# Kernel tuning notes

Hardware: AMD Instinct MI355X
Metric: run time of the kernel (lower is better)

The kernel has to match this reference:

```python
import jax, jax.numpy as jnp
import numpy as np
import math

N_NODES = 50000
N_EDGES = 800000
IN_DIM = 128
OUT_DIM = 64
TIME_DIM = 128


def setup_inputs() -> dict:
    key = jax.random.key(0)
    ks = jax.random.split(key, 9)
    return {
        "node_feats": jax.random.normal(ks[0], (N_NODES, IN_DIM), dtype=jnp.float32),
        "time_diff": jax.random.uniform(ks[1], (N_EDGES,), dtype=jnp.float32),
        "src": jax.random.randint(ks[2], (N_EDGES,), 0, N_NODES, dtype=jnp.int32),
        "dst": jax.random.randint(ks[3], (N_EDGES,), 0, N_NODES, dtype=jnp.int32),
        "W": jax.random.normal(ks[4], (OUT_DIM, IN_DIM), dtype=jnp.float32) * 0.05,
        "Wv": jax.random.normal(ks[5], (OUT_DIM, IN_DIM), dtype=jnp.float32) * 0.05,
        "omega": jax.random.normal(ks[6], (TIME_DIM // 2,), dtype=jnp.float32),
        "Wt": jax.random.normal(ks[7], (OUT_DIM, TIME_DIM), dtype=jnp.float32) * 0.05,
        "a": jax.random.normal(ks[8], (3 * OUT_DIM,), dtype=jnp.float32) * 0.05,
    }


def reference(node_feats, time_diff, src, dst, W, Wv, omega, Wt, a):
    N = node_feats.shape[0]
    d = W.shape[0]  # out_dim
    time_dim = 2 * omega.shape[0]

    # gather + linear projections per edge
    h_src = node_feats[src] @ W.T          # [E, d]
    h_dst = node_feats[dst] @ W.T          # [E, d]
    v_src = node_feats[src] @ Wv.T         # [E, d]

    # temporal encoding: interleaved sin/cos of t * omega, scaled by sqrt(1/dim)
    ang = time_diff[:, None] * omega[None, :]                       # [E, dim/2]
    pe = jnp.stack([jnp.sin(ang), jnp.cos(ang)], axis=-1)
    pe = pe.reshape(ang.shape[0], time_dim) * jnp.float32(math.sqrt(1.0 / time_dim))
    t_emb = pe @ Wt.T                                               # [E, d]

    # attn_fc(concat([h_src, h_dst, t_emb])) == split dot products (same math, no big concat)
    e = h_src @ a[:d] + h_dst @ a[d:2 * d] + t_emb @ a[2 * d:]      # [E]
    e = jnp.where(e > 0, e, 0.2 * e)  # LeakyReLU(0.2)

    # edge_softmax: softmax over incoming edges of each destination node
    m = jax.ops.segment_max(e, dst, num_segments=N)
    ex = jnp.exp(e - m[dst])
    den = jax.ops.segment_sum(ex, dst, num_segments=N)
    alpha = ex / den[dst]  # dropout is identity in eval mode

    # weighted message scatter-sum aggregation
    msg = v_src * alpha[:, None]                                    # [E, d]
    return jax.ops.segment_sum(msg, dst, num_segments=N)            # [N, d]
```

## Files before the change

### kernel.cpp

```cpp
#include <hip/hip_runtime.h>
#include <hip/hip_bf16.h>
#include <hip/hip_fp16.h>
#include <math.h>

#define IN_DIM   128
#define OUT_DIM  64
#define THALF    64
#define PE_SCALE 0.08838834764831845f
#define TBL      2048
#define EPB_LOG  14
#define EPB      (1 << EPB_LOG)

typedef __attribute__((ext_vector_type(8))) short  short8;
typedef __attribute__((ext_vector_type(4))) float  f32x4;

__device__ inline unsigned short bf16_rne(float x) {
    unsigned u = __float_as_uint(x);
    return (unsigned short)((u + 0x7FFFu + ((u >> 16) & 1u)) >> 16);
}

__global__ __launch_bounds__(256) void k_prep(
    const float* __restrict__ W, const float* __restrict__ Wt,
    const float* __restrict__ a, const float* __restrict__ Wv,
    const float* __restrict__ omega,
    float* __restrict__ gtab, unsigned short* __restrict__ Bp,
    int* __restrict__ pref)
{
    __shared__ float satv[IN_DIM];
    __shared__ float saW1[IN_DIM], saW2[IN_DIM];
    int t = threadIdx.x;
    if (t < IN_DIM) {
        float x3 = 0.f;
        for (int j = 0; j < OUT_DIM; ++j)
            x3 += a[2 * OUT_DIM + j] * Wt[j * IN_DIM + t];
        satv[t] = x3;
        if (blockIdx.x == 0) {
            float x1 = 0.f, x2 = 0.f;
            for (int j = 0; j < OUT_DIM; ++j) {
                float wj = W[j * IN_DIM + t];
                x1 += a[j] * wj;
                x2 += a[OUT_DIM + j] * wj;
            }
            saW1[t] = x1; saW2[t] = x2;
        }
    }
    __syncthreads();

    int idx = blockIdx.x * 256 + t;
    if (idx <= TBL) {
        float tt = (float)idx * (1.0f / TBL);
        float acc = 0.f;
#pragma unroll
        for (int i = 0; i < THALF; ++i) {
            float sp, cp;
            __sincosf(tt * omega[i], &sp, &cp);
            acc += sp * satv[2 * i] + cp * satv[2 * i + 1];
        }
        gtab[idx] = acc;
    }
    if (idx < 64) pref[idx] = 0;

    if (blockIdx.x == 0) {
        for (int i = t; i < 5 * 4 * 64 * 8; i += 256) {
            int j    = i & 7;
            int lane = (i >> 3) & 63;
            int k0i  = (i >> 9) & 3;
            int tt   = i >> 11;
            int kk = k0i * 32 + (lane >> 4) * 8 + j;
            int n  = lane & 15;
            float val;
            if (tt < 4)     val = Wv[(tt * 16 + n) * IN_DIM + kk];
            else            val = (n == 0) ? saW1[kk] : (n == 1) ? saW2[kk] : 0.f;
            Bp[i] = bf16_rne(val);
        }
    }
}

__global__ __launch_bounds__(1024) void k_hist_mfma(
    const int* __restrict__ dst,
    unsigned short* __restrict__ lrank,
    unsigned short* __restrict__ ghist16,
    const float* __restrict__ feats,
    const unsigned short* __restrict__ Bp,
    unsigned short* __restrict__ vb,
    float* __restrict__ s1,
    float* __restrict__ s2,
    int N, int E, int B)
{
    extern __shared__ unsigned h[];
    int t = threadIdx.x;
    if ((int)blockIdx.x < B) {
        int NH = (N + 1) >> 1;
        for (int i = t; i < NH; i += 1024) h[i] = 0u;
        __syncthreads();
        int b = blockIdx.x;
        int e0 = b << EPB_LOG;
        int e1 = e0 + EPB; if (e1 > E) e1 = E;
        for (int e = e0 + t; e < e1; e += 1024) {
            int d = dst[e];
            unsigned inc = (d & 1) ? 0x10000u : 1u;
            unsigned old = atomicAdd(&h[d >> 1], inc);
            lrank[e] = (unsigned short)((d & 1) ? (old >> 16) : (old & 0xFFFFu));
        }
        __syncthreads();
        unsigned* gh32 = (unsigned*)(ghist16 + (size_t)b * N);
        for (int w = t; w < NH; w += 1024) gh32[w] = h[w];
        return;
    }
    int gwave = ((int)blockIdx.x - B) * 16 + (t >> 6);
    int lane  = t & 63;
    int ntiles = (N + 15) >> 4;
    if (gwave >= ntiles) return;
    int row = lane & 15, quad = lane >> 4;
    int nodeA = gwave * 16 + row;
    int nodeL = nodeA < N ? nodeA : N - 1;

    const float* arow = feats + (size_t)nodeL * IN_DIM + quad * 8;
    short8 afrag[4];
#pragma unroll
    for (int k0i = 0; k0i < 4; ++k0i) {
        float4 fa = *(const float4*)(arow + k0i * 32);
        float4 fb = *(const float4*)(arow + k0i * 32 + 4);
        union { unsigned u[4]; short8 s; } cv;
        cv.u[0] = (__float_as_uint(fa.x) >> 16) | (__float_as_uint(fa.y) & 0xFFFF0000u);
        cv.u[1] = (__float_as_uint(fa.z) >> 16) | (__float_as_uint(fa.w) & 0xFFFF0000u);
        cv.u[2] = (__float_as_uint(fb.x) >> 16) | (__float_as_uint(fb.y) & 0xFFFF0000u);
        cv.u[3] = (__float_as_uint(fb.z) >> 16) | (__float_as_uint(fb.w) & 0xFFFF0000u);
        afrag[k0i] = cv.s;
    }

    const short8* B8 = (const short8*)Bp;
    f32x4 acc[5];
#pragma unroll
    for (int tt = 0; tt < 5; ++tt) acc[tt] = (f32x4){0.f, 0.f, 0.f, 0.f};
#pragma unroll
    for (int tt = 0; tt < 5; ++tt) {
#pragma unroll
        for (int k0i = 0; k0i < 4; ++k0i)
            acc[tt] = __builtin_amdgcn_mfma_f32_16x16x32_bf16(
                afrag[k0i], B8[(tt * 4 + k0i) * 64 + lane], acc[tt], 0, 0, 0);
    }

    int col = lane & 15;
    int baseNode = gwave * 16 + quad * 4;
#pragma unroll
    for (int r = 0; r < 4; ++r) {
        int nd = baseNode + r;
        if (nd < N) {
            unsigned short* vr = vb + (size_t)nd * OUT_DIM + col;
#pragma unroll
            for (int tt = 0; tt < 4; ++tt) vr[tt * 16] = bf16_rne(acc[tt][r]);
            if (col == 0)      s1[nd] = acc[4][r];
            else if (col == 1) s2[nd] = acc[4][r];
        }
    }
}

__global__ __launch_bounds__(256) void k_scan_fuse(
    unsigned short* __restrict__ ghist16,
    int* __restrict__ offs,
    int* __restrict__ pref,
    int B, int N)
{
    __shared__ int lds[256];
    int b = blockIdx.x, t = threadIdx.x;
    int n0 = b * 1024 + t * 4;
    unsigned r0 = 0, r1 = 0, r2 = 0, r3 = 0;
    if (n0 + 3 < N) {
        for (int bb = 0; bb < B; ++bb) {
            unsigned short* p = ghist16 + (size_t)bb * N + n0;
            uint2 c = *(uint2*)p;
            uint2 w;
            w.x = (r0 & 0xFFFFu) | (r1 << 16);
            w.y = (r2 & 0xFFFFu) | (r3 << 16);
            *(uint2*)p = w;
            r0 += c.x & 0xFFFFu; r1 += c.x >> 16;
            r2 += c.y & 0xFFFFu; r3 += c.y >> 16;
        }
    } else if (n0 < N) {
        for (int bb = 0; bb < B; ++bb) {
            unsigned short* p = ghist16 + (size_t)bb * N + n0;
            unsigned c0 = p[0]; p[0] = (unsigned short)r0; r0 += c0;
            if (n0 + 1 < N) { unsigned c = p[1]; p[1] = (unsigned short)r1; r1 += c; }
            if (n0 + 2 < N) { unsigned c = p[2]; p[2] = (unsigned short)r2; r2 += c; }
            if (n0 + 3 < N) { unsigned c = p[3]; p[3] = (unsigned short)r3; r3 += c; }
        }
    }
    int s = (int)(r0 + r1 + r2 + r3);
    lds[t] = s;
    __syncthreads();
    for (int off = 1; off < 256; off <<= 1) {
        int tmp = (t >= off) ? lds[t - off] : 0;
        __syncthreads();
        lds[t] += tmp;
        __syncthreads();
    }
    int ex = lds[t] - s;
    if (n0 + 3 < N) {
        int4 o;
        o.x = ex;
        o.y = ex + (int)r0;
        o.z = ex + (int)(r0 + r1);
        o.w = ex + (int)(r0 + r1 + r2);
        *(int4*)(offs + n0) = o;
    } else if (n0 < N) {
        offs[n0] = ex;
        if (n0 + 1 < N) offs[n0 + 1] = ex + (int)r0;
        if (n0 + 2 < N) offs[n0 + 2] = ex + (int)(r0 + r1);
        if (n0 + 3 < N) offs[n0 + 3] = ex + (int)(r0 + r1 + r2);
    }
    int total = lds[255];
    if (t > b && t < (int)gridDim.x) atomicAdd(pref + t, total);
}

__global__ __launch_bounds__(256) void k_scatter_fused(
    const float* __restrict__ tdiff,
    const int* __restrict__ src,
    const int* __restrict__ dst,
    const float* __restrict__ gtab,
    const float* __restrict__ s1,
    const float* __restrict__ s2,
    const unsigned short* __restrict__ lrank,
    const unsigned short* __restrict__ ghist16,
    const int* __restrict__ offs,
    const int* __restrict__ pref,
    unsigned* __restrict__ payload,
    int N, int E)
{
    int base = (blockIdx.x * 256 + threadIdx.x) * 8;
    if (base >= E) return;
    if (base + 8 <= E) {
        int4   sa = *(const int4*)(src + base);
        int4   sb = *(const int4*)(src + base + 4);
        int4   da = *(const int4*)(dst + base);
        int4   db = *(const int4*)(dst + base + 4);
        float4 ta = *(const float4*)(tdiff + base);
        float4 tb = *(const float4*)(tdiff + base + 4);
        ushort4 la = *(const ushort4*)(lrank + base);
        ushort4 lb = *(const ushort4*)(lrank + base + 4);
        int s[8]    = {sa.x, sa.y, sa.z, sa.w, sb.x, sb.y, sb.z, sb.w};
        int d[8]    = {da.x, da.y, da.z, da.w, db.x, db.y, db.z, db.w};
        float tv[8] = {ta.x, ta.y, ta.z, ta.w, tb.x, tb.y, tb.z, tb.w};
        int lr[8]   = {la.x, la.y, la.z, la.w, lb.x, lb.y, lb.z, lb.w};

        int pos[8];
#pragma unroll
        for (int i = 0; i < 8; ++i) {
            int b = (base + i) >> EPB_LOG;
            pos[i] = offs[d[i]] + pref[d[i] >> 10] +
                     (int)ghist16[(size_t)b * N + d[i]] + lr[i];
        }
#pragma unroll
        for (int i = 0; i < 8; ++i) {
            float a1 = s1[s[i]];
            float a2 = s2[d[i]];
            float x = tv[i] * (float)TBL;
            int i0 = (int)x;
            i0 = i0 < 0 ? 0 : (i0 > TBL - 1 ? TBL - 1 : i0);
            float fr = x - (float)i0;
            float ev = a1 + a2 + PE_SCALE * (gtab[i0] + fr * (gtab[i0 + 1] - gtab[i0]));
            ev = ev > 0.f ? ev : 0.2f * ev;
            unsigned pw = ((unsigned)s[i] << 16) | (unsigned)__half_as_ushort(__float2half(ev));
            payload[pos[i]] = pw;
        }
    } else {
        for (int e = base; e < E; ++e) {
            int s = src[e], d = dst[e];
            float a1 = s1[s], a2 = s2[d];
            float x = tdiff[e] * (float)TBL;
            int i0 = (int)x;
            i0 = i0 < 0 ? 0 : (i0 > TBL - 1 ? TBL - 1 : i0);
            float fr = x - (float)i0;
            float ev = a1 + a2 + PE_SCALE * (gtab[i0] + fr * (gtab[i0 + 1] - gtab[i0]));
            ev = ev > 0.f ? ev : 0.2f * ev;
            unsigned pw = ((unsigned)s << 16) | (unsigned)__half_as_ushort(__float2half(ev));
            int b = e >> EPB_LOG;
            int pos = offs[d] + pref[d >> 10] + (int)ghist16[(size_t)b * N + d] + (int)lrank[e];
            payload[pos] = pw;
        }
    }
}

__global__ __launch_bounds__(256) void k_aggregate(
    const int* __restrict__ offs,
    const int* __restrict__ pref,
    const unsigned* __restrict__ payload,
    const unsigned short* __restrict__ vb,
    float* __restrict__ out,
    int N, int E)
{
    int gid  = blockIdx.x * 256 + threadIdx.x;
    int node = gid >> 4;
    int l16  = gid & 15;
    if (node >= N) return;
    int beg = offs[node] + pref[node >> 10];
    int end = (node + 1 < N) ? (offs[node + 1] + pref[(node + 1) >> 10]) : E;
    int deg = end - beg;

    float acc0 = 0.f, acc1 = 0.f, acc2 = 0.f, acc3 = 0.f, den = 0.f;
    unsigned plA = (deg > 0) ? payload[beg] : 0u;
    unsigned plB = (deg > 1) ? payload[beg + 1] : 0u;
    for (int j = 0; j < deg; j += 2) {
        unsigned pl0 = plA, pl1 = plB;
        bool v1 = (j + 1 < deg);
        if (j + 2 < deg) plA = payload[beg + j + 2];
        if (j + 3 < deg) plB = payload[beg + j + 3];
        float ex0 = __expf(__half2float(__ushort_as_half((unsigned short)(pl0 & 0xFFFFu))));
        float ex1 = v1 ? __expf(__half2float(__ushort_as_half((unsigned short)(pl1 & 0xFFFFu)))) : 0.f;
        int sv0 = (int)(pl0 >> 16);
        int sv1 = v1 ? (int)(pl1 >> 16) : 0;
        uint2 w0 = *(const uint2*)(vb + (size_t)sv0 * OUT_DIM + l16 * 4);
        uint2 w1 = *(const uint2*)(vb + (size_t)sv1 * OUT_DIM + l16 * 4);
        den  += ex0 + ex1;
        acc0 += ex0 * __uint_as_float(w0.x << 16)         + ex1 * __uint_as_float(w1.x << 16);
        acc1 += ex0 * __uint_as_float(w0.x & 0xFFFF0000u) + ex1 * __uint_as_float(w1.x & 0xFFFF0000u);
        acc2 += ex0 * __uint_as_float(w0.y << 16)         + ex1 * __uint_as_float(w1.y << 16);
        acc3 += ex0 * __uint_as_float(w0.y & 0xFFFF0000u) + ex1 * __uint_as_float(w1.y & 0xFFFF0000u);
    }

    float inv = (deg > 0) ? 1.f / den : 0.f;
    float* o = out + (size_t)node * OUT_DIM + l16 * 4;
    *(float4*)o = make_float4(acc0 * inv, acc1 * inv, acc2 * inv, acc3 * inv);
}

extern "C" void kernel_launch(void* const* d_in, const int* in_sizes, int n_in,
                              void* d_out, int out_size, void* d_ws, size_t ws_size,
                              hipStream_t stream) {
    const float* feats = (const float*)d_in[0];
    const float* tdiff = (const float*)d_in[1];
    const int*   src   = (const int*)d_in[2];
    const int*   dst   = (const int*)d_in[3];
    const float* W     = (const float*)d_in[4];
    const float* Wv    = (const float*)d_in[5];
    const float* omega = (const float*)d_in[6];
    const float* Wt    = (const float*)d_in[7];
    const float* a     = (const float*)d_in[8];
    float* out = (float*)d_out;

    int N = in_sizes[0] / IN_DIM;
    int E = in_sizes[1];
    int B = (E + EPB - 1) >> EPB_LOG;

    float* ws      = (float*)d_ws;
    unsigned short* vb = (unsigned short*)ws;
    float* s1      = ws + (size_t)N * 32;
    float* s2      = s1 + N;
    unsigned* payload = (unsigned*)(s2 + N);
    unsigned short* lrank = (unsigned short*)(payload + E);
    int*   offs    = (int*)(lrank + ((E + 1) & ~1));
    int    offs_elems = ((N + 1023) / 1024) * 1024;
    int*   pref    = offs + offs_elems;
    float* gtab    = (float*)(pref + 64);
    unsigned short* Bp = (unsigned short*)(gtab + TBL + 1);
    size_t gho = ((size_t)((char*)(Bp + 10240) - (char*)ws) + 7) & ~(size_t)7;
    unsigned short* ghist16 = (unsigned short*)((char*)ws + gho);

    int nb = (N + 1023) / 1024;
    int ntiles = (N + 15) / 16;
    int mblocks = (ntiles + 15) / 16;
    int eb8 = (E + 8 * 256 - 1) / (8 * 256);
    unsigned ldsb = (unsigned)(((N + 1) / 2) * 4);

    k_prep<<<(TBL / 256) + 1, 256, 0, stream>>>(W, Wt, a, Wv, omega, gtab, Bp, pref);
    k_hist_mfma<<<B + mblocks, 1024, ldsb, stream>>>(dst, lrank, ghist16,
                                                     feats, Bp, vb, s1, s2, N, E, B);
    k_scan_fuse<<<nb, 256, 0, stream>>>(ghist16, offs, pref, B, N);
    k_scatter_fused<<<eb8, 256, 0, stream>>>(tdiff, src, dst, gtab, s1, s2,
                                             lrank, ghist16, offs, pref, payload, N, E);
    long long aggt = (long long)N * 16;
    k_aggregate<<<(int)((aggt + 255) / 256), 256, 0, stream>>>(offs, pref, payload, vb, out, N, E);
}
```

Measured before the change: 172.2 us.

## Fuse all stages into one cooperative megakernel with grid-wide syncs

Replaces the chain of prep, histogram/MFMA projection, scan, scatter and aggregate launches with a single cooperative kernel of 256 blocks × 1024 threads. The phases are separated by grid.sync, and the node projection MFMA is moved into the scan phase on otherwise idle blocks. The aim is to remove per-launch overhead and inter-kernel gaps. The trade-off is that the scatter and aggregate phases now run at a fixed occupancy of one large-LDS block per CU, which may hide gather latency less well. The original multi-kernel path is kept as a fallback if the cooperative launch fails.

```diff
diff --git a/kernel.cpp b/kernel.cpp
--- a/kernel.cpp
+++ b/kernel.cpp
@@ -1,7 +1,10 @@
 #include <hip/hip_runtime.h>
+#include <hip/hip_cooperative_groups.h>
 #include <hip/hip_bf16.h>
 #include <hip/hip_fp16.h>
 #include <math.h>
+
+namespace cg = cooperative_groups;
 
 #define IN_DIM   128
 #define OUT_DIM  64
@@ -10,6 +13,7 @@
 #define TBL      2048
 #define EPB_LOG  14
 #define EPB      (1 << EPB_LOG)
+#define PREP_BLKS 9
 
 typedef __attribute__((ext_vector_type(8))) short  short8;
 typedef __attribute__((ext_vector_type(4))) float  f32x4;
@@ -17,6 +21,270 @@
 __device__ inline unsigned short bf16_rne(float x) {
     unsigned u = __float_as_uint(x);
     return (unsigned short)((u + 0x7FFFu + ((u >> 16) & 1u)) >> 16);
+}
+
+__global__ __launch_bounds__(1024) void k_mega(
+    const float* __restrict__ W, const float* __restrict__ Wt,
+    const float* __restrict__ a, const float* __restrict__ Wv,
+    const float* __restrict__ omega,
+    float* __restrict__ gtab, unsigned short* __restrict__ Bp,
+    int* __restrict__ pref,
+    const int* __restrict__ dst,
+    unsigned short* __restrict__ lrank,
+    unsigned short* __restrict__ ghist16,
+    const float* __restrict__ feats,
+    unsigned short* __restrict__ vb,
+    float* __restrict__ s1, float* __restrict__ s2,
+    const float* __restrict__ tdiff,
+    const int* __restrict__ src,
+    int* __restrict__ offs,
+    unsigned* __restrict__ payload,
+    float* __restrict__ out,
+    int N, int E, int B, int nb)
+{
+    extern __shared__ unsigned h[];
+    __shared__ float satv[IN_DIM], saW1[IN_DIM], saW2[IN_DIM];
+    cg::grid_group grid = cg::this_grid();
+    int blk = blockIdx.x, t = threadIdx.x;
+
+    if (blk < PREP_BLKS) {
+        if (t < IN_DIM) {
+            float x3 = 0.f;
+            for (int j = 0; j < OUT_DIM; ++j)
+                x3 += a[2 * OUT_DIM + j] * Wt[j * IN_DIM + t];
+            satv[t] = x3;
+            if (blk == 0) {
+                float x1 = 0.f, x2 = 0.f;
+                for (int j = 0; j < OUT_DIM; ++j) {
+                    float wj = W[j * IN_DIM + t];
+                    x1 += a[j] * wj;
+                    x2 += a[OUT_DIM + j] * wj;
+                }
+                saW1[t] = x1; saW2[t] = x2;
+            }
+        }
+        __syncthreads();
+        if (t < 256) {
+            int idx = blk * 256 + t;
+            if (idx <= TBL) {
+                float tt = (float)idx * (1.0f / TBL);
+                float acc = 0.f;
+#pragma unroll
+                for (int i = 0; i < THALF; ++i) {
+                    float sp, cp;
+                    __sincosf(tt * omega[i], &sp, &cp);
+                    acc += sp * satv[2 * i] + cp * satv[2 * i + 1];
+                }
+                gtab[idx] = acc;
+            }
+            if (idx < 64) pref[idx] = 0;
+        }
+        if (blk == 0) {
+            for (int i = t; i < 5 * 4 * 64 * 8; i += 1024) {
+                int j    = i & 7;
+                int lane = (i >> 3) & 63;
+                int k0i  = (i >> 9) & 3;
+                int tt   = i >> 11;
+                int kk = k0i * 32 + (lane >> 4) * 8 + j;
+                int n  = lane & 15;
+                float val;
+                if (tt < 4)     val = Wv[(tt * 16 + n) * IN_DIM + kk];
+                else            val = (n == 0) ? saW1[kk] : (n == 1) ? saW2[kk] : 0.f;
+                Bp[i] = bf16_rne(val);
+            }
+        }
+    } else if (blk < PREP_BLKS + B) {
+        int NH = (N + 1) >> 1;
+        for (int i = t; i < NH; i += 1024) h[i] = 0u;
+        __syncthreads();
+        int b = blk - PREP_BLKS;
+        int e0 = b << EPB_LOG;
+        int e1 = e0 + EPB; if (e1 > E) e1 = E;
+        for (int e = e0 + t; e < e1; e += 1024) {
+            int d = dst[e];
+            unsigned inc = (d & 1) ? 0x10000u : 1u;
+            unsigned old = atomicAdd(&h[d >> 1], inc);
+            lrank[e] = (unsigned short)((d & 1) ? (old >> 16) : (old & 0xFFFFu));
+        }
+        __syncthreads();
+        unsigned* gh32 = (unsigned*)(ghist16 + (size_t)b * N);
+        for (int w = t; w < NH; w += 1024) gh32[w] = h[w];
+    }
+    __threadfence();
+    grid.sync();
+
+    if (blk < nb) {
+        int* lds1k = (int*)h;
+        int n = blk * 1024 + t;
+        unsigned r = 0;
+        if (n < N) {
+            for (int bb = 0; bb < B; ++bb) {
+                unsigned short* p = ghist16 + (size_t)bb * N + n;
+                unsigned c = *p;
+                *p = (unsigned short)r;
+                r += c;
+            }
+        }
+        lds1k[t] = (int)r;
+        __syncthreads();
+        for (int off = 1; off < 1024; off <<= 1) {
+            int tmp = (t >= off) ? lds1k[t - off] : 0;
+            __syncthreads();
+            lds1k[t] += tmp;
+            __syncthreads();
+        }
+        int ex = lds1k[t] - (int)r;
+        if (n < N) offs[n] = ex;
+        int total = lds1k[1023];
+        if (t > blk && t < nb) atomicAdd(pref + t, total);
+    } else {
+        int gwave = (blk - nb) * 16 + (t >> 6);
+        int lane  = t & 63;
+        int ntiles = (N + 15) >> 4;
+        if (gwave < ntiles) {
+            int row = lane & 15, quad = lane >> 4;
+            int nodeA = gwave * 16 + row;
+            int nodeL = nodeA < N ? nodeA : N - 1;
+
+            const float* arow = feats + (size_t)nodeL * IN_DIM + quad * 8;
+            short8 afrag[4];
+#pragma unroll
+            for (int k0i = 0; k0i < 4; ++k0i) {
+                float4 fa = *(const float4*)(arow + k0i * 32);
+                float4 fb = *(const float4*)(arow + k0i * 32 + 4);
+                union { unsigned u[4]; short8 s; } cv;
+                cv.u[0] = (__float_as_uint(fa.x) >> 16) | (__float_as_uint(fa.y) & 0xFFFF0000u);
+                cv.u[1] = (__float_as_uint(fa.z) >> 16) | (__float_as_uint(fa.w) & 0xFFFF0000u);
+                cv.u[2] = (__float_as_uint(fb.x) >> 16) | (__float_as_uint(fb.y) & 0xFFFF0000u);
+                cv.u[3] = (__float_as_uint(fb.z) >> 16) | (__float_as_uint(fb.w) & 0xFFFF0000u);
+                afrag[k0i] = cv.s;
+            }
+
+            const short8* B8 = (const short8*)Bp;
+            f32x4 acc[5];
+#pragma unroll
+            for (int tt = 0; tt < 5; ++tt) acc[tt] = (f32x4){0.f, 0.f, 0.f, 0.f};
+#pragma unroll
+            for (int tt = 0; tt < 5; ++tt) {
+#pragma unroll
+                for (int k0i = 0; k0i < 4; ++k0i)
+                    acc[tt] = __builtin_amdgcn_mfma_f32_16x16x32_bf16(
+                        afrag[k0i], B8[(tt * 4 + k0i) * 64 + lane], acc[tt], 0, 0, 0);
+            }
+
+            int col = lane & 15;
+            int baseNode = gwave * 16 + quad * 4;
+#pragma unroll
+            for (int r = 0; r < 4; ++r) {
+                int nd = baseNode + r;
+                if (nd < N) {
+                    unsigned short* vr = vb + (size_t)nd * OUT_DIM + col;
+#pragma unroll
+                    for (int tt = 0; tt < 4; ++tt) vr[tt * 16] = bf16_rne(acc[tt][r]);
+                    if (col == 0)      s1[nd] = acc[4][r];
+                    else if (col == 1) s2[nd] = acc[4][r];
+                }
+            }
+        }
+    }
+    __threadfence();
+    grid.sync();
+
+    {
+        int tid = blk * 1024 + t;
+        for (int c = tid; c * 8 < E; c += 256 * 1024) {
+            int base = c * 8;
+            if (base + 8 <= E) {
+                int4   sa = *(const int4*)(src + base);
+                int4   sb = *(const int4*)(src + base + 4);
+                int4   da = *(const int4*)(dst + base);
+                int4   db = *(const int4*)(dst + base + 4);
+                float4 ta = *(const float4*)(tdiff + base);
+                float4 tb = *(const float4*)(tdiff + base + 4);
+                ushort4 la = *(const ushort4*)(lrank + base);
+                ushort4 lb = *(const ushort4*)(lrank + base + 4);
+                int s[8]    = {sa.x, sa.y, sa.z, sa.w, sb.x, sb.y, sb.z, sb.w};
+                int d[8]    = {da.x, da.y, da.z, da.w, db.x, db.y, db.z, db.w};
+                float tv[8] = {ta.x, ta.y, ta.z, ta.w, tb.x, tb.y, tb.z, tb.w};
+                int lr[8]   = {la.x, la.y, la.z, la.w, lb.x, lb.y, lb.z, lb.w};
+
+                int pos[8];
+#pragma unroll
+                for (int i = 0; i < 8; ++i) {
+                    int b = (base + i) >> EPB_LOG;
+                    pos[i] = offs[d[i]] + pref[d[i] >> 10] +
+                             (int)ghist16[(size_t)b * N + d[i]] + lr[i];
+                }
+#pragma unroll
+                for (int i = 0; i < 8; ++i) {
+                    float a1 = s1[s[i]];
+                    float a2 = s2[d[i]];
+                    float x = tv[i] * (float)TBL;
+                    int i0 = (int)x;
+                    i0 = i0 < 0 ? 0 : (i0 > TBL - 1 ? TBL - 1 : i0);
+                    float fr = x - (float)i0;
+                    float ev = a1 + a2 + PE_SCALE * (gtab[i0] + fr * (gtab[i0 + 1] - gtab[i0]));
+                    ev = ev > 0.f ? ev : 0.2f * ev;
+                    unsigned pw = ((unsigned)s[i] << 16) | (unsigned)__half_as_ushort(__float2half(ev));
+                    payload[pos[i]] = pw;
+                }
+            } else {
+                for (int e = base; e < E; ++e) {
+                    int s = src[e], d = dst[e];
+                    float a1 = s1[s], a2 = s2[d];
+                    float x = tdiff[e] * (float)TBL;
+                    int i0 = (int)x;
+                    i0 = i0 < 0 ? 0 : (i0 > TBL - 1 ? TBL - 1 : i0);
+                    float fr = x - (float)i0;
+                    float ev = a1 + a2 + PE_SCALE * (gtab[i0] + fr * (gtab[i0 + 1] - gtab[i0]));
+                    ev = ev > 0.f ? ev : 0.2f * ev;
+                    unsigned pw = ((unsigned)s << 16) | (unsigned)__half_as_ushort(__float2half(ev));
+                    int b = e >> EPB_LOG;
+                    int pos = offs[d] + pref[d >> 10] + (int)ghist16[(size_t)b * N + d] + (int)lrank[e];
+                    payload[pos] = pw;
+                }
+            }
+        }
+    }
+    __threadfence();
+    grid.sync();
+
+    {
+        int tid = blk * 1024 + t;
+        int W16 = N * 16;
+        for (int w = tid; w < W16; w += 256 * 1024) {
+            int node = w >> 4;
+            int l16  = w & 15;
+            int beg = offs[node] + pref[node >> 10];
+            int end = (node + 1 < N) ? (offs[node + 1] + pref[(node + 1) >> 10]) : E;
+            int deg = end - beg;
+
+            float acc0 = 0.f, acc1 = 0.f, acc2 = 0.f, acc3 = 0.f, den = 0.f;
+            unsigned plA = (deg > 0) ? payload[beg] : 0u;
+            unsigned plB = (deg > 1) ? payload[beg + 1] : 0u;
+            for (int j = 0; j < deg; j += 2) {
+                unsigned pl0 = plA, pl1 = plB;
+                bool v1 = (j + 1 < deg);
+                if (j + 2 < deg) plA = payload[beg + j + 2];
+                if (j + 3 < deg) plB = payload[beg + j + 3];
+                float ex0 = __expf(__half2float(__ushort_as_half((unsigned short)(pl0 & 0xFFFFu))));
+                float ex1 = v1 ? __expf(__half2float(__ushort_as_half((unsigned short)(pl1 & 0xFFFFu)))) : 0.f;
+                int sv0 = (int)(pl0 >> 16);
+                int sv1 = v1 ? (int)(pl1 >> 16) : 0;
+                uint2 w0 = *(const uint2*)(vb + (size_t)sv0 * OUT_DIM + l16 * 4);
+                uint2 w1 = *(const uint2*)(vb + (size_t)sv1 * OUT_DIM + l16 * 4);
+                den  += ex0 + ex1;
+                acc0 += ex0 * __uint_as_float(w0.x << 16)         + ex1 * __uint_as_float(w1.x << 16);
+                acc1 += ex0 * __uint_as_float(w0.x & 0xFFFF0000u) + ex1 * __uint_as_float(w1.x & 0xFFFF0000u);
+                acc2 += ex0 * __uint_as_float(w0.y << 16)         + ex1 * __uint_as_float(w1.y << 16);
+                acc3 += ex0 * __uint_as_float(w0.y & 0xFFFF0000u) + ex1 * __uint_as_float(w1.y & 0xFFFF0000u);
+            }
+
+            float inv = (deg > 0) ? 1.f / den : 0.f;
+            float* o = out + (size_t)node * OUT_DIM + l16 * 4;
+            *(float4*)o = make_float4(acc0 * inv, acc1 * inv, acc2 * inv, acc3 * inv);
+        }
+    }
 }
 
 __global__ __launch_bounds__(256) void k_prep(
@@ -361,7 +629,19 @@
     int eb8 = (E + 8 * 256 - 1) / (8 * 256);
     unsigned ldsb = (unsigned)(((N + 1) / 2) * 4);
 
-    k_prep<<<(TBL / 256) + 1, 256, 0, stream>>>(W, Wt, a, Wv, omega, gtab, Bp, pref);
+    void* kargs[] = {
+        (void*)&W, (void*)&Wt, (void*)&a, (void*)&Wv, (void*)&omega,
+        (void*)&gtab, (void*)&Bp, (void*)&pref,
+        (void*)&dst, (void*)&lrank, (void*)&ghist16,
+        (void*)&feats, (void*)&vb, (void*)&s1, (void*)&s2,
+        (void*)&tdiff, (void*)&src, (void*)&offs, (void*)&payload,
+        (void*)&out, (void*)&N, (void*)&E, (void*)&B, (void*)&nb
+    };
+    hipError_t err = hipLaunchCooperativeKernel(
+        (const void*)k_mega, dim3(256), dim3(1024), kargs, ldsb, stream);
+    if (err == hipSuccess) return;
+
+    k_prep<<<PREP_BLKS, 256, 0, stream>>>(W, Wt, a, Wv, omega, gtab, Bp, pref);
     k_hist_mfma<<<B + mblocks, 1024, ldsb, stream>>>(dst, lrank, ghist16,
                                                      feats, Bp, vb, s1, s2, N, E, B);
     k_scan_fuse<<<nb, 256, 0, stream>>>(ghist16, offs, pref, B, N);
```

Result: slower. 606.7 us (+252.4%).

## Fuse prep kernel into histogram/MFMA kernel and build B operand in LDS

Applied to the files above, without the earlier changes.

Merges the separate prep kernel into the histogram/MFMA launch. Dedicated blocks build the time-encoding table, and each MFMA block recomputes the packed bf16 weight operand into shared memory instead of reading it from global memory. This removes one kernel launch and its serialization point. In exchange, every MFMA block repeats the small weight-folding and packing work and adds a barrier before its MFMAs.

```diff
diff --git a/kernel.cpp b/kernel.cpp
--- a/kernel.cpp
+++ b/kernel.cpp
@@ -10,6 +10,7 @@
 #define TBL      2048
 #define EPB_LOG  14
 #define EPB      (1 << EPB_LOG)
+#define NGTAB    3
 
 typedef __attribute__((ext_vector_type(8))) short  short8;
 typedef __attribute__((ext_vector_type(4))) float  f32x4;
@@ -19,81 +20,52 @@
     return (unsigned short)((u + 0x7FFFu + ((u >> 16) & 1u)) >> 16);
 }
 
-__global__ __launch_bounds__(256) void k_prep(
+__global__ __launch_bounds__(1024) void k_fused1(
     const float* __restrict__ W, const float* __restrict__ Wt,
     const float* __restrict__ a, const float* __restrict__ Wv,
     const float* __restrict__ omega,
-    float* __restrict__ gtab, unsigned short* __restrict__ Bp,
-    int* __restrict__ pref)
-{
-    __shared__ float satv[IN_DIM];
-    __shared__ float saW1[IN_DIM], saW2[IN_DIM];
-    int t = threadIdx.x;
-    if (t < IN_DIM) {
-        float x3 = 0.f;
-        for (int j = 0; j < OUT_DIM; ++j)
-            x3 += a[2 * OUT_DIM + j] * Wt[j * IN_DIM + t];
-        satv[t] = x3;
-        if (blockIdx.x == 0) {
-            float x1 = 0.f, x2 = 0.f;
-            for (int j = 0; j < OUT_DIM; ++j) {
-                float wj = W[j * IN_DIM + t];
-                x1 += a[j] * wj;
-                x2 += a[OUT_DIM + j] * wj;
-            }
-            saW1[t] = x1; saW2[t] = x2;
-        }
-    }
-    __syncthreads();
-
-    int idx = blockIdx.x * 256 + t;
-    if (idx <= TBL) {
-        float tt = (float)idx * (1.0f / TBL);
-        float acc = 0.f;
-#pragma unroll
-        for (int i = 0; i < THALF; ++i) {
-            float sp, cp;
-            __sincosf(tt * omega[i], &sp, &cp);
-            acc += sp * satv[2 * i] + cp * satv[2 * i + 1];
-        }
-        gtab[idx] = acc;
-    }
-    if (idx < 64) pref[idx] = 0;
-
-    if (blockIdx.x == 0) {
-        for (int i = t; i < 5 * 4 * 64 * 8; i += 256) {
-            int j    = i & 7;
-            int lane = (i >> 3) & 63;
-            int k0i  = (i >> 9) & 3;
-            int tt   = i >> 11;
-            int kk = k0i * 32 + (lane >> 4) * 8 + j;
-            int n  = lane & 15;
-            float val;
-            if (tt < 4)     val = Wv[(tt * 16 + n) * IN_DIM + kk];
-            else            val = (n == 0) ? saW1[kk] : (n == 1) ? saW2[kk] : 0.f;
-            Bp[i] = bf16_rne(val);
-        }
-    }
-}
-
-__global__ __launch_bounds__(1024) void k_hist_mfma(
+    float* __restrict__ gtab, int* __restrict__ pref,
     const int* __restrict__ dst,
     unsigned short* __restrict__ lrank,
     unsigned short* __restrict__ ghist16,
     const float* __restrict__ feats,
-    const unsigned short* __restrict__ Bp,
     unsigned short* __restrict__ vb,
-    float* __restrict__ s1,
-    float* __restrict__ s2,
+    float* __restrict__ s1, float* __restrict__ s2,
     int N, int E, int B)
 {
     extern __shared__ unsigned h[];
+    __shared__ float satv[IN_DIM], saW1[IN_DIM], saW2[IN_DIM];
     int t = threadIdx.x;
-    if ((int)blockIdx.x < B) {
+    int blk = blockIdx.x;
+
+    if (blk < NGTAB) {
+        if (t < IN_DIM) {
+            float x3 = 0.f;
+            for (int j = 0; j < OUT_DIM; ++j)
+                x3 += a[2 * OUT_DIM + j] * Wt[j * IN_DIM + t];
+            satv[t] = x3;
+        }
+        __syncthreads();
+        int idx = blk * 1024 + t;
+        if (idx <= TBL) {
+            float tt = (float)idx * (1.0f / TBL);
+            float acc = 0.f;
+#pragma unroll
+            for (int i = 0; i < THALF; ++i) {
+                float sp, cp;
+                __sincosf(tt * omega[i], &sp, &cp);
+                acc += sp * satv[2 * i] + cp * satv[2 * i + 1];
+            }
+            gtab[idx] = acc;
+        }
+        if (idx < 64) pref[idx] = 0;
+        return;
+    }
+    if (blk < NGTAB + B) {
         int NH = (N + 1) >> 1;
         for (int i = t; i < NH; i += 1024) h[i] = 0u;
         __syncthreads();
-        int b = blockIdx.x;
+        int b = blk - NGTAB;
         int e0 = b << EPB_LOG;
         int e1 = e0 + EPB; if (e1 > E) e1 = E;
         for (int e = e0 + t; e < e1; e += 1024) {
@@ -107,7 +79,33 @@
         for (int w = t; w < NH; w += 1024) gh32[w] = h[w];
         return;
     }
-    int gwave = ((int)blockIdx.x - B) * 16 + (t >> 6);
+
+    unsigned short* lBp = (unsigned short*)h;
+    if (t < IN_DIM) {
+        float x1 = 0.f, x2 = 0.f;
+        for (int j = 0; j < OUT_DIM; ++j) {
+            float wj = W[j * IN_DIM + t];
+            x1 += a[j] * wj;
+            x2 += a[OUT_DIM + j] * wj;
+        }
+        saW1[t] = x1; saW2[t] = x2;
+    }
+    __syncthreads();
+    for (int i = t; i < 5 * 4 * 64 * 8; i += 1024) {
+        int j    = i & 7;
+        int lane = (i >> 3) & 63;
+        int k0i  = (i >> 9) & 3;
+        int tt   = i >> 11;
+        int kk = k0i * 32 + (lane >> 4) * 8 + j;
+        int n  = lane & 15;
+        float val;
+        if (tt < 4)     val = Wv[(tt * 16 + n) * IN_DIM + kk];
+        else            val = (n == 0) ? saW1[kk] : (n == 1) ? saW2[kk] : 0.f;
+        lBp[i] = bf16_rne(val);
+    }
+    __syncthreads();
+
+    int gwave = (blk - NGTAB - B) * 16 + (t >> 6);
     int lane  = t & 63;
     int ntiles = (N + 15) >> 4;
     if (gwave >= ntiles) return;
@@ -129,7 +127,7 @@
         afrag[k0i] = cv.s;
     }
 
-    const short8* B8 = (const short8*)Bp;
+    const short8* B8 = (const short8*)lBp;
     f32x4 acc[5];
 #pragma unroll
     for (int tt = 0; tt < 5; ++tt) acc[tt] = (f32x4){0.f, 0.f, 0.f, 0.f};
@@ -351,8 +349,7 @@
     int    offs_elems = ((N + 1023) / 1024) * 1024;
     int*   pref    = offs + offs_elems;
     float* gtab    = (float*)(pref + 64);
-    unsigned short* Bp = (unsigned short*)(gtab + TBL + 1);
-    size_t gho = ((size_t)((char*)(Bp + 10240) - (char*)ws) + 7) & ~(size_t)7;
+    size_t gho = ((size_t)((char*)(gtab + TBL + 1) - (char*)ws) + 7) & ~(size_t)7;
     unsigned short* ghist16 = (unsigned short*)((char*)ws + gho);
 
     int nb = (N + 1023) / 1024;
@@ -361,9 +358,9 @@
     int eb8 = (E + 8 * 256 - 1) / (8 * 256);
     unsigned ldsb = (unsigned)(((N + 1) / 2) * 4);
 
-    k_prep<<<(TBL / 256) + 1, 256, 0, stream>>>(W, Wt, a, Wv, omega, gtab, Bp, pref);
-    k_hist_mfma<<<B + mblocks, 1024, ldsb, stream>>>(dst, lrank, ghist16,
-                                                     feats, Bp, vb, s1, s2, N, E, B);
+    k_fused1<<<NGTAB + B + mblocks, 1024, ldsb, stream>>>(
+        W, Wt, a, Wv, omega, gtab, pref,
+        dst, lrank, ghist16, feats, vb, s1, s2, N, E, B);
     k_scan_fuse<<<nb, 256, 0, stream>>>(ghist16, offs, pref, B, N);
     k_scatter_fused<<<eb8, 256, 0, stream>>>(tdiff, src, dst, gtab, s1, s2,
                                              lrank, ghist16, offs, pref, payload, N, E);
```

Result: faster. 158.1 us (-8.2%).
